# Kernel optimization log

Measured on AMD Instinct MI355X. Metric: run time of the kernel, lower is better.

The kernel has to match this reference:

```python
import jax, jax.numpy as jnp
import numpy as np

N_NODES = 50000
N_EDGES = 800000
IN_DIM, HID, HEADS = 3, 64, 4
NEG_SLOPE = 0.2  # PyG GATConv default leaky_relu slope


def _glorot(key, shape):
    fan_in, fan_out = shape[0], shape[-1]
    lim = (6.0 / (fan_in + fan_out)) ** 0.5
    return jax.random.uniform(key, shape, jnp.float32, -lim, lim)


def setup_inputs() -> dict:
    key = jax.random.key(0)
    ks = jax.random.split(key, 12)
    x = jax.random.normal(ks[0], (N_NODES, IN_DIM), jnp.float32)
    edge_index = jax.random.randint(ks[1], (2, N_EDGES), 0, N_NODES, jnp.int64)
    return {
        "x": x,
        "edge_index": edge_index,
        "W1": _glorot(ks[2], (IN_DIM, HEADS * HID)),
        "a_src1": _glorot(ks[3], (HEADS, HID)),
        "a_dst1": _glorot(ks[4], (HEADS, HID)),
        "b1": jnp.zeros((HEADS * HID,), jnp.float32),
        "W2": _glorot(ks[5], (HEADS * HID, HID)),
        "a_src2": _glorot(ks[6], (1, HID)),
        "a_dst2": _glorot(ks[7], (1, HID)),
        "b2": jnp.zeros((HID,), jnp.float32),
        # fc: 64 -> 1
        "Wfc": _glorot(ks[8], (HID, 1)),
        "bfc": jnp.zeros((1,), jnp.float32),
    }


def _gat_layer(x, src, dst, W, a_src, a_dst, b, heads, out_ch, n):
    # h: [N, H, C]
    h = (x @ W).reshape(n, heads, out_ch)
    # per-node attention halves, gathered per edge -> [E, H]
    alpha_s = jnp.einsum("nhc,hc->nh", h, a_src)
    alpha_d = jnp.einsum("nhc,hc->nh", h, a_dst)
    e = jax.nn.leaky_relu(alpha_s[src] + alpha_d[dst], NEG_SLOPE)
    # numerically stable segment softmax over incoming edges of each dst node
    e_max = jax.ops.segment_max(e, dst, num_segments=n)
    ex = jnp.exp(e - e_max[dst])
    denom = jax.ops.segment_sum(ex, dst, num_segments=n)
    alpha = ex / (denom[dst] + 1e-16)  # [E, H]
    # weighted scatter-aggregate of source features
    msg = h[src] * alpha[:, :, None]  # [E, H, C]
    out = jax.ops.segment_sum(msg, dst, num_segments=n)  # [N, H, C]
    return out.reshape(n, heads * out_ch) + b


def reference(x, edge_index, W1, a_src1, a_dst1, b1, W2, a_src2, a_dst2, b2, Wfc, bfc):
    n = x.shape[0]
    # PyG GATConv adds self-loops by default
    loops = jnp.arange(n, dtype=edge_index.dtype)
    src = jnp.concatenate([edge_index[0], loops])
    dst = jnp.concatenate([edge_index[1], loops])
    # dropout layers are identity in eval mode
    h = _gat_layer(x, src, dst, W1, a_src1, a_dst1, b1, HEADS, HID, n)
    h = jax.nn.elu(h)
    h = _gat_layer(h, src, dst, W2, a_src2, a_dst2, b2, 1, HID, n)
    h = jax.nn.elu(h)
    out = jax.nn.sigmoid(h @ Wfc + bfc)
    return out.squeeze(-1)
```

## Files before the change

### kernel.cpp

```cpp
#include <hip/hip_runtime.h>
#include <hip/hip_fp16.h>
#include <math.h>

#define N_NODES 50000
#define N_EDGES 800000
#define E_TOT   (N_EDGES + N_NODES)
#define NEG_SLOPE 0.2f
#define NSLICE 8
#define NODES_PER_SLICE (N_NODES / NSLICE)
#define SLICE_BLOCKS 256

#define CNT_OFF    0UL
#define CSR_OFF    200000UL
#define VAS2_OFF   6600000UL
#define VAD2_OFF   6601024UL
#define PK1_OFF    6602048UL
#define AD1_OFF    8202048UL
#define X2_OFF     9002048UL
#define H2_OFF     34602048UL
#define AS2_OFF    41002048UL
#define AD2_OFF    41202048UL

__device__ __forceinline__ float wave_reduce_sum(float v) {
    #pragma unroll
    for (int off = 32; off > 0; off >>= 1) v += __shfl_xor(v, off, 64);
    return v;
}
__device__ __forceinline__ float grp_reduce_sum(float v) {
    #pragma unroll
    for (int off = 8; off > 0; off >>= 1) v += __shfl_xor(v, off, 64);
    return v;
}
__device__ __forceinline__ float lrelu(float v) { return v > 0.f ? v : NEG_SLOPE * v; }
__device__ __forceinline__ float elu(float v)   { return v > 0.f ? v : __expf(v) - 1.f; }

__global__ void node_alpha1(const float* __restrict__ x, const float* __restrict__ W1,
                            const float* __restrict__ a_s1, const float* __restrict__ a_d1,
                            const float* __restrict__ W2, const float* __restrict__ a_s2,
                            const float* __restrict__ a_d2,
                            float* __restrict__ pk1, float* __restrict__ ad1,
                            unsigned* __restrict__ cnt,
                            float* __restrict__ vas2, float* __restrict__ vad2) {
    __shared__ float svs[12], svd[12];
    int t = threadIdx.x, h = t >> 6, lane = t & 63;
    float avs = a_s1[h*64 + lane], avd = a_d1[h*64 + lane];
    #pragma unroll
    for (int k = 0; k < 3; ++k) {
        float w = W1[k*256 + h*64 + lane];
        float ps = wave_reduce_sum(w * avs);
        float pd = wave_reduce_sum(w * avd);
        if (lane == 0) { svs[k*4+h] = ps; svd[k*4+h] = pd; }
    }
    if (blockIdx.x < 64) {
        int k = blockIdx.x*4 + h;
        float wv = W2[k*64 + lane];
        float ps2 = wave_reduce_sum(wv * a_s2[lane]);
        float pd2 = wave_reduce_sum(wv * a_d2[lane]);
        if (lane == 0) { vas2[k] = ps2; vad2[k] = pd2; }
    }
    __syncthreads();
    int n = blockIdx.x*256 + t;
    if (n >= N_NODES) return;
    cnt[n] = 0u;
    float x0 = x[n*3+0], x1 = x[n*3+1], x2v = x[n*3+2];
    float4 s, d;
    s.x = x0*svs[0] + x1*svs[4] + x2v*svs[8];
    s.y = x0*svs[1] + x1*svs[5] + x2v*svs[9];
    s.z = x0*svs[2] + x1*svs[6] + x2v*svs[10];
    s.w = x0*svs[3] + x1*svs[7] + x2v*svs[11];
    d.x = x0*svd[0] + x1*svd[4] + x2v*svd[8];
    d.y = x0*svd[1] + x1*svd[5] + x2v*svd[9];
    d.z = x0*svd[2] + x1*svd[6] + x2v*svd[10];
    d.w = x0*svd[3] + x1*svd[7] + x2v*svd[11];
    float4* pp = (float4*)(pk1 + (size_t)n*8);
    pp[0] = s;
    pp[1] = make_float4(x0, x1, x2v, 0.f);
    *(float4*)(ad1 + (size_t)n*4) = d;
}

__global__ void build_csr(const int* __restrict__ ei, unsigned* __restrict__ cnt,
                          unsigned short* __restrict__ csr) {
    int slice = blockIdx.x & (NSLICE-1);
    int bi    = blockIdx.x >> 3;
    int lo = slice * NODES_PER_SLICE, hi = lo + NODES_PER_SLICE;
    const int stride = SLICE_BLOCKS * 256;
    for (int c = bi*256 + threadIdx.x; c < N_EDGES/4; c += stride) {
        const long long* pd = (const long long*)(ei + N_EDGES + c*4);
        long long da = __builtin_nontemporal_load(pd);
        long long db = __builtin_nontemporal_load(pd + 1);
        const long long* ps = (const long long*)(ei + c*4);
        long long sa = __builtin_nontemporal_load(ps);
        long long sb = __builtin_nontemporal_load(ps + 1);
        int dd[4] = {(int)da, (int)(da >> 32), (int)db, (int)(db >> 32)};
        int ss[4] = {(int)sa, (int)(sa >> 32), (int)sb, (int)(sb >> 32)};
        #pragma unroll
        for (int i = 0; i < 4; ++i) {
            if (dd[i] >= lo && dd[i] < hi) {
                unsigned p = atomicAdd(&cnt[dd[i]], 1u);
                if (p < 64u) csr[((size_t)dd[i] << 6) + p] = (unsigned short)ss[i];
            }
        }
    }
    for (int v = lo + bi*256 + threadIdx.x; v < hi; v += stride) {
        unsigned p = atomicAdd(&cnt[v], 1u);
        if (p < 64u) csr[((size_t)v << 6) + p] = (unsigned short)v;
    }
}

__global__ void gat1_node(const unsigned short* __restrict__ csr, const unsigned* __restrict__ cnt,
                          const float* __restrict__ pk1, const float* __restrict__ W1,
                          const float* __restrict__ ad1, const float* __restrict__ b1,
                          __half* __restrict__ x2out) {
    int lane = threadIdx.x & 63, w = threadIdx.x >> 6;
    int subl = lane & 15, grp = lane >> 4;
    int n = blockIdx.x*16 + w*4 + grp;
    unsigned deg = min(cnt[n], 64u);
    const unsigned short* row = csr + ((size_t)n << 6);
    float4 adv = *(const float4*)(ad1 + (size_t)n*4);
    float d0=0.f, d1=0.f, d2=0.f, d3=0.f;
    float g00=0,g01=0,g02=0, g10=0,g11=0,g12=0, g20=0,g21=0,g22=0, g30=0,g31=0,g32=0;
    for (unsigned c = subl; c < deg; c += 16) {
        int s = row[c];
        const float4* pp = (const float4*)(pk1 + (size_t)s*8);
        float4 as = pp[0];
        float4 xv = pp[1];
        float e0 = __expf(lrelu(as.x+adv.x));
        float e1 = __expf(lrelu(as.y+adv.y));
        float e2 = __expf(lrelu(as.z+adv.z));
        float e3 = __expf(lrelu(as.w+adv.w));
        d0 += e0; d1 += e1; d2 += e2; d3 += e3;
        g00 = fmaf(e0,xv.x,g00); g01 = fmaf(e0,xv.y,g01); g02 = fmaf(e0,xv.z,g02);
        g10 = fmaf(e1,xv.x,g10); g11 = fmaf(e1,xv.y,g11); g12 = fmaf(e1,xv.z,g12);
        g20 = fmaf(e2,xv.x,g20); g21 = fmaf(e2,xv.y,g21); g22 = fmaf(e2,xv.z,g22);
        g30 = fmaf(e3,xv.x,g30); g31 = fmaf(e3,xv.y,g31); g32 = fmaf(e3,xv.z,g32);
    }
    float r_0 = 1.f/(grp_reduce_sum(d0) + 1e-16f);
    float r_1 = 1.f/(grp_reduce_sum(d1) + 1e-16f);
    float r_2 = 1.f/(grp_reduce_sum(d2) + 1e-16f);
    float r_3 = 1.f/(grp_reduce_sum(d3) + 1e-16f);
    g00 = grp_reduce_sum(g00)*r_0; g01 = grp_reduce_sum(g01)*r_0; g02 = grp_reduce_sum(g02)*r_0;
    g10 = grp_reduce_sum(g10)*r_1; g11 = grp_reduce_sum(g11)*r_1; g12 = grp_reduce_sum(g12)*r_1;
    g20 = grp_reduce_sum(g20)*r_2; g21 = grp_reduce_sum(g21)*r_2; g22 = grp_reduce_sum(g22)*r_2;
    g30 = grp_reduce_sum(g30)*r_3; g31 = grp_reduce_sum(g31)*r_3; g32 = grp_reduce_sum(g32)*r_3;
    __half* xrow = x2out + (size_t)n*256;
    #pragma unroll
    for (int i = 0; i < 16; ++i) {
        int j = i*16 + subl;
        float ga, gb, gc;
        if      (i < 4)  { ga=g00; gb=g01; gc=g02; }
        else if (i < 8)  { ga=g10; gb=g11; gc=g12; }
        else if (i < 12) { ga=g20; gb=g21; gc=g22; }
        else             { ga=g30; gb=g31; gc=g32; }
        float val = ga*W1[j] + gb*W1[256+j] + gc*W1[512+j] + b1[j];
        xrow[j] = __float2half(elu(val));
    }
}

#define KB 32
__global__ __launch_bounds__(256) void node_prep2(
        const __half* __restrict__ x2, const float* __restrict__ W2,
        const float* __restrict__ vas2, const float* __restrict__ vad2,
        __half* __restrict__ h2, float* __restrict__ as2, float* __restrict__ ad2) {
    __shared__ float xT[KB][68];
    __shared__ float Wt[KB][64];
    int t = threadIdx.x;
    int n0 = blockIdx.x * 64;
    int i = t & 15, j = t >> 4;
    int snode = t >> 2, g8 = t & 3;
    int snr = n0 + snode; if (snr >= N_NODES) snr = N_NODES - 1;
    float acc[4][4] = {{0,0,0,0},{0,0,0,0},{0,0,0,0},{0,0,0,0}};
    float pas = 0.f, pad = 0.f;
    for (int k0 = 0; k0 < 256; k0 += KB) {
        __syncthreads();
        {
            float4 raw = *(const float4*)(x2 + (size_t)snr*256 + k0 + g8*8);
            const __half2* hp = (const __half2*)&raw;
            #pragma unroll
            for (int q = 0; q < 4; ++q) {
                float2 f = __half22float2(hp[q]);
                int kk = g8*8 + 2*q;
                xT[kk+0][snode] = f.x;
                xT[kk+1][snode] = f.y;
                pas = fmaf(f.x, vas2[k0+kk],   pas);
                pas = fmaf(f.y, vas2[k0+kk+1], pas);
                pad = fmaf(f.x, vad2[k0+kk],   pad);
                pad = fmaf(f.y, vad2[k0+kk+1], pad);
            }
        }
        int p = t;
        #pragma unroll
        for (int rr = 0; rr < 2; ++rr, p += 256) {
            int kr = p >> 4, c4 = p & 15;
            *(float4*)(&Wt[kr][c4*4]) = *(const float4*)(W2 + (size_t)(k0+kr)*64 + c4*4);
        }
        __syncthreads();
        #pragma unroll
        for (int k = 0; k < KB; ++k) {
            float4 xv = *(const float4*)(&xT[k][4*i]);
            float4 wv = *(const float4*)(&Wt[k][4*j]);
            acc[0][0]=fmaf(xv.x,wv.x,acc[0][0]); acc[0][1]=fmaf(xv.x,wv.y,acc[0][1]);
            acc[0][2]=fmaf(xv.x,wv.z,acc[0][2]); acc[0][3]=fmaf(xv.x,wv.w,acc[0][3]);
            acc[1][0]=fmaf(xv.y,wv.x,acc[1][0]); acc[1][1]=fmaf(xv.y,wv.y,acc[1][1]);
            acc[1][2]=fmaf(xv.y,wv.z,acc[1][2]); acc[1][3]=fmaf(xv.y,wv.w,acc[1][3]);
            acc[2][0]=fmaf(xv.z,wv.x,acc[2][0]); acc[2][1]=fmaf(xv.z,wv.y,acc[2][1]);
            acc[2][2]=fmaf(xv.z,wv.z,acc[2][2]); acc[2][3]=fmaf(xv.z,wv.w,acc[2][3]);
            acc[3][0]=fmaf(xv.w,wv.x,acc[3][0]); acc[3][1]=fmaf(xv.w,wv.y,acc[3][1]);
            acc[3][2]=fmaf(xv.w,wv.z,acc[3][2]); acc[3][3]=fmaf(xv.w,wv.w,acc[3][3]);
        }
    }
    pas += __shfl_xor(pas, 1, 64); pas += __shfl_xor(pas, 2, 64);
    pad += __shfl_xor(pad, 1, 64); pad += __shfl_xor(pad, 2, 64);
    if (g8 == 0 && n0 + snode < N_NODES) { as2[n0+snode] = pas; ad2[n0+snode] = pad; }
    #pragma unroll
    for (int ii = 0; ii < 4; ++ii) {
        int n = n0 + 4*i + ii;
        if (n < N_NODES) {
            union { __half2 h[2]; float2 f; } u;
            u.h[0] = __floats2half2_rn(acc[ii][0], acc[ii][1]);
            u.h[1] = __floats2half2_rn(acc[ii][2], acc[ii][3]);
            *(float2*)(h2 + (size_t)n*64 + 4*j) = u.f;
        }
    }
}

__global__ void gat2_node(const unsigned short* __restrict__ csr, const unsigned* __restrict__ cnt,
                          const __half* __restrict__ h2, const float* __restrict__ as2,
                          const float* __restrict__ ad2, const float* __restrict__ b2,
                          const float* __restrict__ Wfc, const float* __restrict__ bfc,
                          float* __restrict__ out) {
    int lane = threadIdx.x & 63, w = threadIdx.x >> 6;
    int n = blockIdx.x*4 + w;
    unsigned deg = min(cnt[n], 64u);
    const unsigned short* row = csr + ((size_t)n << 6);
    float adv = ad2[n];
    int s_l = 0; float ex_l = 0.f;
    if (lane < (int)deg) {
        s_l = row[lane];
        ex_l = __expf(lrelu(as2[s_l] + adv));
    }
    float den = wave_reduce_sum(ex_l);
    float acc = 0.f;
    unsigned degr = (deg + 7u) & ~7u;
    for (unsigned c = 0; c < degr; c += 8) {
        #pragma unroll
        for (int u = 0; u < 8; ++u) {
            int e = (int)c + u;
            float ex = __shfl(ex_l, e, 64);
            int   s  = __shfl(s_l,  e, 64);
            float hv = __half2float(h2[((size_t)s << 6) + lane]);
            acc = fmaf(hv, ex, acc);
        }
    }
    float v = elu(acc/(den + 1e-16f) + b2[lane]);
    float part = wave_reduce_sum(v * Wfc[lane]);
    if (lane == 0) out[n] = 1.f/(1.f + __expf(-(part + bfc[0])));
}

extern "C" void kernel_launch(void* const* d_in, const int* in_sizes, int n_in,
                              void* d_out, int out_size, void* d_ws, size_t ws_size,
                              hipStream_t stream) {
    const float* x      = (const float*)d_in[0];
    const int*   ei     = (const int*)  d_in[1];
    const float* W1     = (const float*)d_in[2];
    const float* a_src1 = (const float*)d_in[3];
    const float* a_dst1 = (const float*)d_in[4];
    const float* b1     = (const float*)d_in[5];
    const float* W2     = (const float*)d_in[6];
    const float* a_src2 = (const float*)d_in[7];
    const float* a_dst2 = (const float*)d_in[8];
    const float* b2     = (const float*)d_in[9];
    const float* Wfc    = (const float*)d_in[10];
    const float* bfc    = (const float*)d_in[11];
    float* out = (float*)d_out;

    char* ws = (char*)d_ws;
    unsigned*       cnt  = (unsigned*)      (ws + CNT_OFF);
    unsigned short* csr  = (unsigned short*)(ws + CSR_OFF);
    float*          vas2 = (float*)         (ws + VAS2_OFF);
    float*          vad2 = (float*)         (ws + VAD2_OFF);
    float*          pk1  = (float*)         (ws + PK1_OFF);
    float*          ad1  = (float*)         (ws + AD1_OFF);
    __half*         x2   = (__half*)        (ws + X2_OFF);
    __half*         h2   = (__half*)        (ws + H2_OFF);
    float*          as2  = (float*)         (ws + AS2_OFF);
    float*          ad2  = (float*)         (ws + AD2_OFF);

    const int BLK = 256;
    node_alpha1 <<<(N_NODES + BLK - 1)/BLK, BLK, 0, stream>>>(
        x, W1, a_src1, a_dst1, W2, a_src2, a_dst2, pk1, ad1, cnt, vas2, vad2);
    build_csr   <<<NSLICE*SLICE_BLOCKS, BLK, 0, stream>>>(ei, cnt, csr);
    gat1_node   <<<N_NODES/16, BLK, 0, stream>>>(csr, cnt, pk1, W1, ad1, b1, x2);
    node_prep2  <<<(N_NODES + 63)/64, BLK, 0, stream>>>(x2, W2, vas2, vad2, h2, as2, ad2);
    gat2_node   <<<N_NODES/4, BLK, 0, stream>>>(csr, cnt, h2, as2, ad2, b2, Wfc, bfc, out);
}
```

Before: 130.6 us.

## Replace sliced CSR build with single-pass edge bucketing plus per-slice scatter

Previously each of the 8 destination slices re-read the whole edge list and kept only its own edges. Now one kernel reads the edges once, bins them by slice in shared memory, and appends packed (dst offset, src) words to global per-slice buckets. A second kernel then scatters each bucket into the CSR with slice-local atomics. This removes the 8x redundant edge reads, at the cost of an extra launch, an extra bucket write and read, and a fallback path for local buffer overflow.

```diff
diff --git a/kernel.cpp b/kernel.cpp
--- a/kernel.cpp
+++ b/kernel.cpp
@@ -8,7 +8,10 @@
 #define NEG_SLOPE 0.2f
 #define NSLICE 8
 #define NODES_PER_SLICE (N_NODES / NSLICE)
-#define SLICE_BLOCKS 256
+#define B_EDGES 1024
+#define LCAP 512
+#define BUCKET_CAP 131072
+#define SLICE_BLOCKS_B 128
 
 #define CNT_OFF    0UL
 #define CSR_OFF    200000UL
@@ -20,6 +23,8 @@
 #define H2_OFF     34602048UL
 #define AS2_OFF    41002048UL
 #define AD2_OFF    41202048UL
+#define GCNT_OFF   41402048UL
+#define GB_OFF     41402112UL
 
 __device__ __forceinline__ float wave_reduce_sum(float v) {
     #pragma unroll
@@ -39,7 +44,7 @@
                             const float* __restrict__ W2, const float* __restrict__ a_s2,
                             const float* __restrict__ a_d2,
                             float* __restrict__ pk1, float* __restrict__ ad1,
-                            unsigned* __restrict__ cnt,
+                            unsigned* __restrict__ cnt, unsigned* __restrict__ gcnt,
                             float* __restrict__ vas2, float* __restrict__ vad2) {
     __shared__ float svs[12], svd[12];
     int t = threadIdx.x, h = t >> 6, lane = t & 63;
@@ -58,6 +63,7 @@
         float pd2 = wave_reduce_sum(wv * a_d2[lane]);
         if (lane == 0) { vas2[k] = ps2; vad2[k] = pd2; }
     }
+    if (blockIdx.x == 64 && t < NSLICE) gcnt[t] = 0u;
     __syncthreads();
     int n = blockIdx.x*256 + t;
     if (n >= N_NODES) return;
@@ -78,29 +84,66 @@
     *(float4*)(ad1 + (size_t)n*4) = d;
 }
 
-__global__ void build_csr(const int* __restrict__ ei, unsigned* __restrict__ cnt,
-                          unsigned short* __restrict__ csr) {
+__global__ __launch_bounds__(256) void bucket_edges(
+        const int* __restrict__ ei, unsigned* __restrict__ gcnt,
+        unsigned* __restrict__ gbucket, unsigned* __restrict__ cnt,
+        unsigned short* __restrict__ csr) {
+    __shared__ unsigned buf[NSLICE][LCAP];
+    __shared__ unsigned bcnt[NSLICE], bbase[NSLICE];
+    int t = threadIdx.x;
+    if (t < NSLICE) bcnt[t] = 0u;
+    __syncthreads();
+    int e0 = blockIdx.x * B_EDGES + t * 4;
+    if (e0 < N_EDGES) {
+        int4 s4 = *(const int4*)(ei + e0);
+        int4 d4 = *(const int4*)(ei + N_EDGES + e0);
+        int ss[4] = {s4.x, s4.y, s4.z, s4.w};
+        int dd[4] = {d4.x, d4.y, d4.z, d4.w};
+        #pragma unroll
+        for (int i = 0; i < 4; ++i) {
+            int slice = dd[i] / NODES_PER_SLICE;
+            unsigned doff = (unsigned)(dd[i] - slice*NODES_PER_SLICE);
+            unsigned p = atomicAdd(&bcnt[slice], 1u);
+            if (p < LCAP) buf[slice][p] = (doff << 16) | (unsigned)ss[i];
+            else {
+                unsigned q = atomicAdd(&cnt[dd[i]], 1u);
+                if (q < 64u) csr[((size_t)dd[i] << 6) + q] = (unsigned short)ss[i];
+            }
+        }
+    }
+    __syncthreads();
+    if (t < NSLICE) {
+        unsigned c = min(bcnt[t], (unsigned)LCAP);
+        bcnt[t] = c;
+        bbase[t] = atomicAdd(&gcnt[t], c);
+    }
+    __syncthreads();
+    #pragma unroll
+    for (int s = 0; s < NSLICE; ++s) {
+        unsigned c = bcnt[s], b = bbase[s];
+        for (unsigned i = t; i < c; i += 256) {
+            unsigned pos = b + i;
+            if (pos < BUCKET_CAP) gbucket[(size_t)s*BUCKET_CAP + pos] = buf[s][i];
+        }
+    }
+}
+
+__global__ void scatter_bucket(const unsigned* __restrict__ gcnt,
+                               const unsigned* __restrict__ gbucket,
+                               unsigned* __restrict__ cnt, unsigned short* __restrict__ csr) {
     int slice = blockIdx.x & (NSLICE-1);
     int bi    = blockIdx.x >> 3;
-    int lo = slice * NODES_PER_SLICE, hi = lo + NODES_PER_SLICE;
-    const int stride = SLICE_BLOCKS * 256;
-    for (int c = bi*256 + threadIdx.x; c < N_EDGES/4; c += stride) {
-        const long long* pd = (const long long*)(ei + N_EDGES + c*4);
-        long long da = __builtin_nontemporal_load(pd);
-        long long db = __builtin_nontemporal_load(pd + 1);
-        const long long* ps = (const long long*)(ei + c*4);
-        long long sa = __builtin_nontemporal_load(ps);
-        long long sb = __builtin_nontemporal_load(ps + 1);
-        int dd[4] = {(int)da, (int)(da >> 32), (int)db, (int)(db >> 32)};
-        int ss[4] = {(int)sa, (int)(sa >> 32), (int)sb, (int)(sb >> 32)};
-        #pragma unroll
-        for (int i = 0; i < 4; ++i) {
-            if (dd[i] >= lo && dd[i] < hi) {
-                unsigned p = atomicAdd(&cnt[dd[i]], 1u);
-                if (p < 64u) csr[((size_t)dd[i] << 6) + p] = (unsigned short)ss[i];
-            }
-        }
-    }
+    int lo = slice * NODES_PER_SLICE;
+    unsigned total = min(gcnt[slice], (unsigned)BUCKET_CAP);
+    const unsigned* bk = gbucket + (size_t)slice*BUCKET_CAP;
+    const int stride = SLICE_BLOCKS_B * 256;
+    for (unsigned i = bi*256 + threadIdx.x; i < total; i += (unsigned)stride) {
+        unsigned e = bk[i];
+        int dst = lo + (int)(e >> 16);
+        unsigned p = atomicAdd(&cnt[dst], 1u);
+        if (p < 64u) csr[((size_t)dst << 6) + p] = (unsigned short)(e & 0xFFFFu);
+    }
+    int hi = lo + NODES_PER_SLICE;
     for (int v = lo + bi*256 + threadIdx.x; v < hi; v += stride) {
         unsigned p = atomicAdd(&cnt[v], 1u);
         if (p < 64u) csr[((size_t)v << 6) + p] = (unsigned short)v;
@@ -284,12 +327,15 @@
     __half*         h2   = (__half*)        (ws + H2_OFF);
     float*          as2  = (float*)         (ws + AS2_OFF);
     float*          ad2  = (float*)         (ws + AD2_OFF);
+    unsigned*       gcnt = (unsigned*)      (ws + GCNT_OFF);
+    unsigned*       gbkt = (unsigned*)      (ws + GB_OFF);
 
     const int BLK = 256;
-    node_alpha1 <<<(N_NODES + BLK - 1)/BLK, BLK, 0, stream>>>(
-        x, W1, a_src1, a_dst1, W2, a_src2, a_dst2, pk1, ad1, cnt, vas2, vad2);
-    build_csr   <<<NSLICE*SLICE_BLOCKS, BLK, 0, stream>>>(ei, cnt, csr);
-    gat1_node   <<<N_NODES/16, BLK, 0, stream>>>(csr, cnt, pk1, W1, ad1, b1, x2);
-    node_prep2  <<<(N_NODES + 63)/64, BLK, 0, stream>>>(x2, W2, vas2, vad2, h2, as2, ad2);
-    gat2_node   <<<N_NODES/4, BLK, 0, stream>>>(csr, cnt, h2, as2, ad2, b2, Wfc, bfc, out);
-}
+    node_alpha1   <<<(N_NODES + BLK - 1)/BLK, BLK, 0, stream>>>(
+        x, W1, a_src1, a_dst1, W2, a_src2, a_dst2, pk1, ad1, cnt, gcnt, vas2, vad2);
+    bucket_edges  <<<(N_EDGES + B_EDGES - 1)/B_EDGES, BLK, 0, stream>>>(ei, gcnt, gbkt, cnt, csr);
+    scatter_bucket<<<NSLICE*SLICE_BLOCKS_B, BLK, 0, stream>>>(gcnt, gbkt, cnt, csr);
+    gat1_node     <<<N_NODES/16, BLK, 0, stream>>>(csr, cnt, pk1, W1, ad1, b1, x2);
+    node_prep2    <<<(N_NODES + 63)/64, BLK, 0, stream>>>(x2, W2, vas2, vad2, h2, as2, ad2);
+    gat2_node     <<<N_NODES/4, BLK, 0, stream>>>(csr, cnt, h2, as2, ad2, b2, Wfc, bfc, out);
+}
```

Measured after the change: 137.3 us. 5.1% more time.
